# Kernel optimization log

Hardware: AMD Instinct MI355X
Metric: run time of the kernel (lower is better)

Reference implementation:

```python
import jax, jax.numpy as jnp
import numpy as np

NUM_HEADS = 12

def setup_inputs() -> dict:
    key = jax.random.key(0)
    ks = jax.random.split(key, 6)
    B, N, C, P = 16, 785, 768, 48
    return {
        "x": jax.random.normal(ks[0], (B, N, C), jnp.float32),
        "qkv_w": jax.random.normal(ks[1], (3 * C, C), jnp.float32) * 0.02,
        "pos_emb": jax.random.normal(ks[2], (N, N, P), jnp.float32) * 0.02,
        "pos_proj_w": jax.random.normal(ks[3], (NUM_HEADS, P), jnp.float32) * 0.02,
        "proj_w": jax.random.normal(ks[4], (C, C), jnp.float32) * 0.02,
        "proj_b": jnp.zeros((C,), jnp.float32),
    }

def reference(x, qkv_w, pos_emb, pos_proj_w, proj_w, proj_b):
    B, N, C = x.shape
    H = NUM_HEADS
    hd = C // H
    scale = hd ** -0.5
    # qkv projection: [B,N,3C] -> q,k,v each [B,H,N,hd]
    qkv = (x @ qkv_w.T).reshape(B, N, 3, H, hd)
    qkv = jnp.transpose(qkv, (2, 0, 3, 1, 4))
    q, k, v = qkv[0], qkv[1], qkv[2]
    # learned relative-position bias: [H,N,N]
    pos_score = jnp.einsum('nmp,hp->hnm', pos_emb, pos_proj_w)
    # attention scores: scale applied AFTER adding bias (matches original)
    attn = (jnp.einsum('bhnd,bhmd->bhnm', q, k) + pos_score[None]) * scale
    attn = jax.nn.softmax(attn, axis=-1)
    out = jnp.einsum('bhnm,bhmd->bhnd', attn, v)
    out = jnp.transpose(out, (0, 2, 1, 3)).reshape(B, N, C)
    return out @ proj_w.T + proj_b
```

## Files before the change

### kernel.cpp

```cpp
#include <hip/hip_runtime.h>
#include <hip/hip_fp16.h>

#define B_ 16
#define N_ 785
#define C_ 768
#define H_ 12
#define HD_ 64
#define P_ 48
#define M_ (B_*N_)
#define POSW 832
#define VTW  832
#define SLOG2E 0.1803368801111244f

#define OFF_Q   0
#define OFF_K   9646080
#define OFF_VT  19292160
#define OFF_POS 29515776
#define OFF_XF  37353216
#define OFF_AO  OFF_XF
#define OFF_WQ  47085312
#define OFF_WP  48854784

struct __align__(16) Half8 { __half h[8]; };
typedef _Float16 half8_t __attribute__((ext_vector_type(8)));
typedef _Float16 half4_t __attribute__((ext_vector_type(4)));
typedef float f32x4 __attribute__((ext_vector_type(4)));

__device__ __forceinline__ void gl16(const void* g, void* l) {
    __builtin_amdgcn_global_load_lds(
        (const __attribute__((address_space(1))) void*)g,
        (__attribute__((address_space(3))) void*)l, 16, 0, 0);
}

__device__ __forceinline__ int xcd_swz(int o, int nwg) {
    const int q = nwg >> 3, r = nwg & 7;
    const int xcd = o & 7, idx = o >> 3;
    const int base = xcd < r ? xcd * (q + 1) : r * (q + 1) + (xcd - r) * q;
    return base + idx;
}

#define NX4 2411520
#define NQ4 442368
#define NP4 147456
#define NTOT4 (NX4+NQ4+NP4)

__global__ __launch_bounds__(256) void convert_f16(
    const float* __restrict__ x, const float* __restrict__ wq,
    const float* __restrict__ wp, _Float16* __restrict__ xo,
    _Float16* __restrict__ wqo, _Float16* __restrict__ wpo)
{
    int i = blockIdx.x * 256 + threadIdx.x;
    const float4* s; _Float16* d; int o;
    if (i < NX4)            { s = (const float4*)x;  d = xo;  o = i; }
    else if (i < NX4 + NQ4) { s = (const float4*)wq; d = wqo; o = i - NX4; }
    else                    { s = (const float4*)wp; d = wpo; o = i - NX4 - NQ4; }
    float4 v = s[o];
    half4_t h = { (_Float16)v.x, (_Float16)v.y, (_Float16)v.z, (_Float16)v.w };
    *(half4_t*)&d[o * 4] = h;
}

#define QKV_NWG (18 * 99)

__global__ __launch_bounds__(256) void qkv_gemm_mfma(
    const _Float16* __restrict__ A, const _Float16* __restrict__ Bw,
    __half* __restrict__ qh, __half* __restrict__ kh, __half* __restrict__ vth)
{
    __shared__ _Float16 Asl[2][128 * 32];
    __shared__ _Float16 Bsl[2][128 * 32];

    const int t  = threadIdx.x;
    const int w  = t >> 6;
    const int l  = t & 63;
    const int lr = l & 15;
    const int lg = l >> 4;
    const int wm = (w >> 1) * 64;
    const int wn = (w & 1) * 64;

    const int g  = xcd_swz(blockIdx.x, QKV_NWG);
    const int nt = g % 18;
    const int n0 = nt * 128;
    const int m0 = (g / 18) * 128;

    const int f1 = t + 256;
    const int ar0 = t >> 2,  ac0 = (t & 3) * 8;
    const int ar1 = f1 >> 2, ac1 = (f1 & 3) * 8;
    const _Float16* Ag0 = A  + (size_t)(m0 + ar0) * 768 + ac0;
    const _Float16* Ag1 = A  + (size_t)(m0 + ar1) * 768 + ac1;
    const _Float16* Bg0 = Bw + (size_t)(n0 + ar0) * 768 + ac0;
    const _Float16* Bg1 = Bw + (size_t)(n0 + ar1) * 768 + ac1;

    f32x4 acc[4][4];
    #pragma unroll
    for (int i = 0; i < 4; ++i)
        #pragma unroll
        for (int j = 0; j < 4; ++j) acc[i][j] = (f32x4){0.f, 0.f, 0.f, 0.f};

    gl16(Ag0, &Asl[0][t * 8]); gl16(Ag1, &Asl[0][f1 * 8]);
    gl16(Bg0, &Bsl[0][t * 8]); gl16(Bg1, &Bsl[0][f1 * 8]);
    __syncthreads();

    #pragma unroll 2
    for (int it = 0; it < 24; ++it) {
        const int cur = it & 1;
        if (it < 23) {
            const int kn = (it + 1) * 32;
            gl16(Ag0 + kn, &Asl[cur ^ 1][t * 8]); gl16(Ag1 + kn, &Asl[cur ^ 1][f1 * 8]);
            gl16(Bg0 + kn, &Bsl[cur ^ 1][t * 8]); gl16(Bg1 + kn, &Bsl[cur ^ 1][f1 * 8]);
        }
        half8_t af[4], bf[4];
        #pragma unroll
        for (int i = 0; i < 4; ++i)
            af[i] = *(const half8_t*)&Asl[cur][(wm + i * 16 + lr) * 32 + lg * 8];
        #pragma unroll
        for (int j = 0; j < 4; ++j)
            bf[j] = *(const half8_t*)&Bsl[cur][(wn + j * 16 + lr) * 32 + lg * 8];
        __builtin_amdgcn_s_setprio(1);
        #pragma unroll
        for (int i = 0; i < 4; ++i)
            #pragma unroll
            for (int j = 0; j < 4; ++j)
                acc[i][j] = __builtin_amdgcn_mfma_f32_16x16x32_f16(af[i], bf[j], acc[i][j], 0, 0, 0);
        __builtin_amdgcn_s_setprio(0);
        __syncthreads();
    }

    const int tsel  = nt / 6;
    const int nbase = n0 - tsel * 768;
    #pragma unroll
    for (int i = 0; i < 4; ++i) {
        #pragma unroll
        for (int r = 0; r < 4; ++r) {
            const int m = m0 + wm + i * 16 + lg * 4 + r;
            if (m >= M_) continue;
            const int bb = m / N_, nn = m - bb * N_;
            #pragma unroll
            for (int j = 0; j < 4; ++j) {
                const int nsec = nbase + wn + j * 16 + lr;
                const int hh = nsec >> 6, dd = nsec & 63;
                const float v = acc[i][j][r];
                if (tsel == 0)
                    qh[((size_t)(bb * H_ + hh) * N_ + nn) * HD_ + dd] = __float2half(v * SLOG2E);
                else if (tsel == 1)
                    kh[((size_t)(bb * H_ + hh) * N_ + nn) * HD_ + dd] = __float2half(v);
                else
                    vth[((size_t)(bb * H_ + hh) * HD_ + dd) * VTW + nn] = __float2half(v);
            }
        }
    }
}

__global__ __launch_bounds__(256) void pos_kernel(
    const float* __restrict__ pe, const float* __restrict__ pw,
    __half* __restrict__ posh)
{
    __shared__ float W[H_][P_];
    const int t = threadIdx.x;
    for (int i = t; i < H_ * P_; i += 256) W[i / P_][i % P_] = pw[i];
    __syncthreads();
    int nm = blockIdx.x * 256 + t;
    if (nm >= N_ * N_) return;
    float e[48];
    const float4* src = (const float4*)(pe + (size_t)nm * 48);
    #pragma unroll
    for (int i = 0; i < 12; ++i) {
        float4 v = src[i];
        e[4*i] = v.x; e[4*i+1] = v.y; e[4*i+2] = v.z; e[4*i+3] = v.w;
    }
    int n = nm / N_, m = nm - n * N_;
    #pragma unroll
    for (int hh = 0; hh < H_; ++hh) {
        float s = 0.f;
        #pragma unroll
        for (int p = 0; p < 48; ++p) s = fmaf(e[p], W[hh][p], s);
        posh[((size_t)hh * N_ + n) * POSW + m] = __float2half(s * SLOG2E);
    }
}

#define NQT 13
#define ATT_NWG (192 * NQT)

__global__ __launch_bounds__(256) void attn_mfma(
    const _Float16* __restrict__ qh, const _Float16* __restrict__ kh,
    const _Float16* __restrict__ vt, const _Float16* __restrict__ posh,
    _Float16* __restrict__ aoh)
{
    __shared__ _Float16 Kl[64][72];
    __shared__ _Float16 Vl[64][72];
    __shared__ _Float16 Bl[64][72];

    const int t  = threadIdx.x;
    const int w  = t >> 6;
    const int l  = t & 63;
    const int lr = l & 15;
    const int lg = l >> 4;

    const int g2   = xcd_swz(blockIdx.x, ATT_NWG);
    const int qt   = g2 % NQT;
    const int rest = g2 / NQT;
    const int b    = rest & 15;
    const int h    = rest >> 4;
    const int bh   = b * H_ + h;
    const int n0   = qt * 64;

    const int qrow = n0 + w * 16 + lr;
    const int qrc  = qrow < N_ ? qrow : N_ - 1;
    const _Float16* qbase = qh + ((size_t)bh * N_ + qrc) * HD_;
    const half8_t qf0 = *(const half8_t*)(qbase + lg * 8);
    const half8_t qf1 = *(const half8_t*)(qbase + 32 + lg * 8);

    f32x4 O0 = {0.f,0.f,0.f,0.f}, O1 = O0, O2 = O0, O3 = O0;
    float m_run = -1e30f;
    float l_run = 0.f;

    const int srow = t >> 2;
    const int scol = (t & 3) * 16;
    const _Float16* kRow = kh + ((size_t)bh * N_) * HD_ + scol;
    const _Float16* vRow = vt + ((size_t)bh * HD_ + srow) * VTW + scol;
    const _Float16* bRow = posh + ((size_t)h * N_ + (n0 + srow < N_ ? n0 + srow : N_ - 1)) * POSW + scol;

    half8_t rk0, rk1, rv0, rv1, rb0, rb1;
    {
        const int gm = srow < N_ ? srow : N_ - 1;
        const half8_t* ks = (const half8_t*)(kRow + (size_t)gm * HD_);
        rk0 = ks[0]; rk1 = ks[1];
        const half8_t* vs = (const half8_t*)vRow;
        rv0 = vs[0]; rv1 = vs[1];
        const half8_t* bs = (const half8_t*)bRow;
        rb0 = bs[0]; rb1 = bs[1];
    }

    for (int c = 0; c < 13; ++c) {
        *(half8_t*)&Kl[srow][scol]     = rk0;
        *(half8_t*)&Kl[srow][scol + 8] = rk1;
        *(half8_t*)&Vl[srow][scol]     = rv0;
        *(half8_t*)&Vl[srow][scol + 8] = rv1;
        *(half8_t*)&Bl[srow][scol]     = rb0;
        *(half8_t*)&Bl[srow][scol + 8] = rb1;
        __syncthreads();

        if (c < 12) {
            const int m0n = (c + 1) * 64;
            const int gm  = (m0n + srow) < N_ ? (m0n + srow) : N_ - 1;
            const half8_t* ks = (const half8_t*)(kRow + (size_t)gm * HD_);
            rk0 = ks[0]; rk1 = ks[1];
            const half8_t* vs = (const half8_t*)(vRow + m0n);
            rv0 = vs[0]; rv1 = vs[1];
            const half8_t* bs = (const half8_t*)(bRow + m0n);
            rb0 = bs[0]; rb1 = bs[1];
        }

        f32x4 s[4];
        __builtin_amdgcn_s_setprio(1);
        #pragma unroll
        for (int ms = 0; ms < 4; ++ms) {
            half4_t b4 = *(const half4_t*)&Bl[w * 16 + lr][ms * 16 + lg * 4];
            f32x4 acc = { (float)b4[0], (float)b4[1], (float)b4[2], (float)b4[3] };
            half8_t k0 = *(const half8_t*)&Kl[ms * 16 + lr][lg * 8];
            half8_t k1 = *(const half8_t*)&Kl[ms * 16 + lr][32 + lg * 8];
            acc = __builtin_amdgcn_mfma_f32_16x16x32_f16(k0, qf0, acc, 0, 0, 0);
            acc = __builtin_amdgcn_mfma_f32_16x16x32_f16(k1, qf1, acc, 0, 0, 0);
            s[ms] = acc;
        }
        __builtin_amdgcn_s_setprio(0);

        if (c == 12) {
            #pragma unroll
            for (int ms = 0; ms < 4; ++ms)
                #pragma unroll
                for (int r = 0; r < 4; ++r)
                    if (ms * 16 + lg * 4 + r >= 17) s[ms][r] = -1e30f;
        }

        float x0 = fmaxf(fmaxf(s[0][0], s[0][1]), s[0][2]);
        float x1 = fmaxf(fmaxf(s[0][3], s[1][0]), s[1][1]);
        float x2 = fmaxf(fmaxf(s[1][2], s[1][3]), s[2][0]);
        float x3 = fmaxf(fmaxf(s[2][1], s[2][2]), s[2][3]);
        float x4 = fmaxf(fmaxf(s[3][0], s[3][1]), s[3][2]);
        float smax = fmaxf(fmaxf(fmaxf(x0, x1), x2),
                           fmaxf(fmaxf(x3, x4), s[3][3]));
        smax = fmaxf(smax, __shfl_xor(smax, 16));
        smax = fmaxf(smax, __shfl_xor(smax, 32));

        if (__any(smax > m_run + 8.f)) {
            const float mn    = fmaxf(m_run, smax);
            const float alpha = exp2f(m_run - mn);
            m_run = mn;
            l_run *= alpha;
            const float a0 = __shfl(alpha, lg * 4 + 0);
            const float a1 = __shfl(alpha, lg * 4 + 1);
            const float a2 = __shfl(alpha, lg * 4 + 2);
            const float a3 = __shfl(alpha, lg * 4 + 3);
            O0[0]*=a0; O0[1]*=a1; O0[2]*=a2; O0[3]*=a3;
            O1[0]*=a0; O1[1]*=a1; O1[2]*=a2; O1[3]*=a3;
            O2[0]*=a0; O2[1]*=a1; O2[2]*=a2; O2[3]*=a3;
            O3[0]*=a0; O3[1]*=a1; O3[2]*=a2; O3[3]*=a3;
        }

        float p[4][4];
        float psum = 0.f;
        #pragma unroll
        for (int ms = 0; ms < 4; ++ms)
            #pragma unroll
            for (int r = 0; r < 4; ++r) {
                p[ms][r] = exp2f(s[ms][r] - m_run);
                psum += p[ms][r];
            }
        psum += __shfl_xor(psum, 16);
        psum += __shfl_xor(psum, 32);
        l_run += psum;

        half8_t pa0 = { (_Float16)p[0][0], (_Float16)p[0][1], (_Float16)p[0][2], (_Float16)p[0][3],
                        (_Float16)p[1][0], (_Float16)p[1][1], (_Float16)p[1][2], (_Float16)p[1][3] };
        half8_t pa1 = { (_Float16)p[2][0], (_Float16)p[2][1], (_Float16)p[2][2], (_Float16)p[2][3],
                        (_Float16)p[3][0], (_Float16)p[3][1], (_Float16)p[3][2], (_Float16)p[3][3] };

        __builtin_amdgcn_s_setprio(1);
        #pragma unroll
        for (int ds = 0; ds < 4; ++ds) {
            const _Float16* vr = &Vl[ds * 16 + lr][0];
            half4_t v00 = *(const half4_t*)&vr[lg * 4];
            half4_t v01 = *(const half4_t*)&vr[16 + lg * 4];
            half4_t v10 = *(const half4_t*)&vr[32 + lg * 4];
            half4_t v11 = *(const half4_t*)&vr[48 + lg * 4];
            half8_t vf0 = __builtin_shufflevector(v00, v01, 0, 1, 2, 3, 4, 5, 6, 7);
            half8_t vf1 = __builtin_shufflevector(v10, v11, 0, 1, 2, 3, 4, 5, 6, 7);
            f32x4& Od = (ds == 0 ? O0 : ds == 1 ? O1 : ds == 2 ? O2 : O3);
            Od = __builtin_amdgcn_mfma_f32_16x16x32_f16(pa0, vf0, Od, 0, 0, 0);
            Od = __builtin_amdgcn_mfma_f32_16x16x32_f16(pa1, vf1, Od, 0, 0, 0);
        }
        __builtin_amdgcn_s_setprio(0);
        __syncthreads();
    }

    const int bb = bh / H_;
    #pragma unroll
    for (int r = 0; r < 4; ++r) {
        const int n = n0 + w * 16 + lg * 4 + r;
        if (n >= N_) continue;
        const float lv  = __shfl(l_run, lg * 4 + r);
        const float inv = 1.f / lv;
        _Float16* dst = aoh + ((size_t)(bb * N_ + n)) * C_ + h * HD_;
        dst[0 * 16 + lr] = (_Float16)(O0[r] * inv);
        dst[1 * 16 + lr] = (_Float16)(O1[r] * inv);
        dst[2 * 16 + lr] = (_Float16)(O2[r] * inv);
        dst[3 * 16 + lr] = (_Float16)(O3[r] * inv);
    }
}

#define PROJ_NWG (6 * 99)

__global__ __launch_bounds__(256) void proj_gemm_mfma(
    const _Float16* __restrict__ A, const _Float16* __restrict__ Bw,
    const float* __restrict__ bias, float* __restrict__ out)
{
    __shared__ _Float16 Asl[2][128 * 32];
    __shared__ _Float16 Bsl[2][128 * 32];

    const int t  = threadIdx.x;
    const int w  = t >> 6;
    const int l  = t & 63;
    const int lr = l & 15;
    const int lg = l >> 4;
    const int wm = (w >> 1) * 64;
    const int wn = (w & 1) * 64;

    const int g  = xcd_swz(blockIdx.x, PROJ_NWG);
    const int n0 = (g % 6) * 128;
    const int m0 = (g / 6) * 128;

    const int f1 = t + 256;
    const int ar0 = t >> 2,  ac0 = (t & 3) * 8;
    const int ar1 = f1 >> 2, ac1 = (f1 & 3) * 8;
    const _Float16* Ag0 = A  + (size_t)(m0 + ar0) * 768 + ac0;
    const _Float16* Ag1 = A  + (size_t)(m0 + ar1) * 768 + ac1;
    const _Float16* Bg0 = Bw + (size_t)(n0 + ar0) * 768 + ac0;
    const _Float16* Bg1 = Bw + (size_t)(n0 + ar1) * 768 + ac1;

    f32x4 acc[4][4];
    #pragma unroll
    for (int i = 0; i < 4; ++i)
        #pragma unroll
        for (int j = 0; j < 4; ++j) acc[i][j] = (f32x4){0.f, 0.f, 0.f, 0.f};

    gl16(Ag0, &Asl[0][t * 8]); gl16(Ag1, &Asl[0][f1 * 8]);
    gl16(Bg0, &Bsl[0][t * 8]); gl16(Bg1, &Bsl[0][f1 * 8]);
    __syncthreads();

    #pragma unroll 2
    for (int it = 0; it < 24; ++it) {
        const int cur = it & 1;
        if (it < 23) {
            const int kn = (it + 1) * 32;
            gl16(Ag0 + kn, &Asl[cur ^ 1][t * 8]); gl16(Ag1 + kn, &Asl[cur ^ 1][f1 * 8]);
            gl16(Bg0 + kn, &Bsl[cur ^ 1][t * 8]); gl16(Bg1 + kn, &Bsl[cur ^ 1][f1 * 8]);
        }
        half8_t af[4], bf[4];
        #pragma unroll
        for (int i = 0; i < 4; ++i)
            af[i] = *(const half8_t*)&Asl[cur][(wm + i * 16 + lr) * 32 + lg * 8];
        #pragma unroll
        for (int j = 0; j < 4; ++j)
            bf[j] = *(const half8_t*)&Bsl[cur][(wn + j * 16 + lr) * 32 + lg * 8];
        __builtin_amdgcn_s_setprio(1);
        #pragma unroll
        for (int i = 0; i < 4; ++i)
            #pragma unroll
            for (int j = 0; j < 4; ++j)
                acc[i][j] = __builtin_amdgcn_mfma_f32_16x16x32_f16(af[i], bf[j], acc[i][j], 0, 0, 0);
        __builtin_amdgcn_s_setprio(0);
        __syncthreads();
    }

    float bj[4];
    #pragma unroll
    for (int j = 0; j < 4; ++j) bj[j] = bias[n0 + wn + j * 16 + lr];
    #pragma unroll
    for (int i = 0; i < 4; ++i) {
        #pragma unroll
        for (int r = 0; r < 4; ++r) {
            const int m = m0 + wm + i * 16 + lg * 4 + r;
            if (m >= M_) continue;
            #pragma unroll
            for (int j = 0; j < 4; ++j) {
                const int n = n0 + wn + j * 16 + lr;
                out[(size_t)m * 768 + n] = acc[i][j][r] + bj[j];
            }
        }
    }
}

extern "C" void kernel_launch(void* const* d_in, const int* in_sizes, int n_in,
                              void* d_out, int out_size, void* d_ws, size_t ws_size,
                              hipStream_t stream)
{
    const float* x     = (const float*)d_in[0];
    const float* qkv_w = (const float*)d_in[1];
    const float* pe    = (const float*)d_in[2];
    const float* pw    = (const float*)d_in[3];
    const float* pjw   = (const float*)d_in[4];
    const float* pjb   = (const float*)d_in[5];
    float* out = (float*)d_out;

    _Float16* wsh  = (_Float16*)d_ws;
    _Float16* qh   = wsh + OFF_Q;
    _Float16* kh   = wsh + OFF_K;
    _Float16* vth  = wsh + OFF_VT;
    _Float16* posh = wsh + OFF_POS;
    _Float16* xf   = wsh + OFF_XF;
    _Float16* aoh  = wsh + OFF_AO;
    _Float16* wqf  = wsh + OFF_WQ;
    _Float16* wpf  = wsh + OFF_WP;

    convert_f16<<<dim3(NTOT4 / 256), 256, 0, stream>>>(x, qkv_w, pjw, xf, wqf, wpf);
    qkv_gemm_mfma<<<dim3(QKV_NWG), 256, 0, stream>>>(
        xf, wqf, (__half*)qh, (__half*)kh, (__half*)vth);
    pos_kernel<<<dim3((N_ * N_ + 255) / 256), 256, 0, stream>>>(pe, pw, (__half*)posh);
    attn_mfma<<<dim3(ATT_NWG), 256, 0, stream>>>(qh, kh, vth, posh, aoh);
    proj_gemm_mfma<<<dim3(PROJ_NWG), 256, 0, stream>>>(aoh, wpf, pjb, out);
}
```

Measured before the change: 275.6 us.

## Split attention key tiles across waves and store V row-major

Reorganizes the attention kernel so each wave handles a 16-key slice of every 64-key tile for all 64 queries, rather than 16 queries against all keys. Each wave keeps its own softmax max and sum plus partial outputs, and these are merged at the end through shared memory with per-wave rescaling and serialized accumulation. V is now written in row-major [bh,N,hd] layout instead of transposed, which removes the strided transposed stores in the QKV GEMM epilogue. The cost is more accumulator registers, strided scalar LDS reads for the V fragments, use of the smaller 16x16x16 MFMA, and an extra cross-wave reduction pass.

```diff
diff --git a/kernel.cpp b/kernel.cpp
--- a/kernel.cpp
+++ b/kernel.cpp
@@ -9,12 +9,11 @@
 #define P_ 48
 #define M_ (B_*N_)
 #define POSW 832
-#define VTW  832
 #define SLOG2E 0.1803368801111244f
 
 #define OFF_Q   0
 #define OFF_K   9646080
-#define OFF_VT  19292160
+#define OFF_V   19292160
 #define OFF_POS 29515776
 #define OFF_XF  37353216
 #define OFF_AO  OFF_XF
@@ -63,7 +62,7 @@
 
 __global__ __launch_bounds__(256) void qkv_gemm_mfma(
     const _Float16* __restrict__ A, const _Float16* __restrict__ Bw,
-    __half* __restrict__ qh, __half* __restrict__ kh, __half* __restrict__ vth)
+    __half* __restrict__ qh, __half* __restrict__ kh, __half* __restrict__ vh)
 {
     __shared__ _Float16 Asl[2][128 * 32];
     __shared__ _Float16 Bsl[2][128 * 32];
@@ -138,12 +137,10 @@
                 const int nsec = nbase + wn + j * 16 + lr;
                 const int hh = nsec >> 6, dd = nsec & 63;
                 const float v = acc[i][j][r];
-                if (tsel == 0)
-                    qh[((size_t)(bb * H_ + hh) * N_ + nn) * HD_ + dd] = __float2half(v * SLOG2E);
-                else if (tsel == 1)
-                    kh[((size_t)(bb * H_ + hh) * N_ + nn) * HD_ + dd] = __float2half(v);
-                else
-                    vth[((size_t)(bb * H_ + hh) * HD_ + dd) * VTW + nn] = __float2half(v);
+                const size_t dst = ((size_t)(bb * H_ + hh) * N_ + nn) * HD_ + dd;
+                if (tsel == 0)      qh[dst] = __float2half(v * SLOG2E);
+                else if (tsel == 1) kh[dst] = __float2half(v);
+                else                vh[dst] = __float2half(v);
             }
         }
     }
@@ -181,12 +178,16 @@
 
 __global__ __launch_bounds__(256) void attn_mfma(
     const _Float16* __restrict__ qh, const _Float16* __restrict__ kh,
-    const _Float16* __restrict__ vt, const _Float16* __restrict__ posh,
+    const _Float16* __restrict__ vh, const _Float16* __restrict__ posh,
     _Float16* __restrict__ aoh)
 {
-    __shared__ _Float16 Kl[64][72];
-    __shared__ _Float16 Vl[64][72];
-    __shared__ _Float16 Bl[64][72];
+    __shared__ __align__(16) char smem[28672];
+    _Float16 (*Kl)[72] = (_Float16 (*)[72])(smem);
+    _Float16 (*Vl)[72] = (_Float16 (*)[72])(smem + 9216);
+    _Float16 (*Bl)[72] = (_Float16 (*)[72])(smem + 18432);
+    float    (*Ol)[68] = (float (*)[68])(smem);
+    float*    Ml       = (float*)(smem + 17408);
+    float*    Ll       = (float*)(smem + 18432);
 
     const int t  = threadIdx.x;
     const int w  = t >> 6;
@@ -202,28 +203,35 @@
     const int bh   = b * H_ + h;
     const int n0   = qt * 64;
 
-    const int qrow = n0 + w * 16 + lr;
-    const int qrc  = qrow < N_ ? qrow : N_ - 1;
-    const _Float16* qbase = qh + ((size_t)bh * N_ + qrc) * HD_;
-    const half8_t qf0 = *(const half8_t*)(qbase + lg * 8);
-    const half8_t qf1 = *(const half8_t*)(qbase + 32 + lg * 8);
-
-    f32x4 O0 = {0.f,0.f,0.f,0.f}, O1 = O0, O2 = O0, O3 = O0;
-    float m_run = -1e30f;
-    float l_run = 0.f;
+    half8_t Qf0[4], Qf1[4];
+    #pragma unroll
+    for (int qg = 0; qg < 4; ++qg) {
+        const int qr = min(n0 + qg * 16 + lr, N_ - 1);
+        const _Float16* qb = qh + ((size_t)bh * N_ + qr) * HD_;
+        Qf0[qg] = *(const half8_t*)(qb + lg * 8);
+        Qf1[qg] = *(const half8_t*)(qb + 32 + lg * 8);
+    }
+
+    f32x4 O[4][4];
+    #pragma unroll
+    for (int qg = 0; qg < 4; ++qg)
+        #pragma unroll
+        for (int ds = 0; ds < 4; ++ds) O[qg][ds] = (f32x4){0.f, 0.f, 0.f, 0.f};
+    float m_r[4] = {-1e30f, -1e30f, -1e30f, -1e30f};
+    float lp[4]  = {0.f, 0.f, 0.f, 0.f};
 
     const int srow = t >> 2;
     const int scol = (t & 3) * 16;
     const _Float16* kRow = kh + ((size_t)bh * N_) * HD_ + scol;
-    const _Float16* vRow = vt + ((size_t)bh * HD_ + srow) * VTW + scol;
-    const _Float16* bRow = posh + ((size_t)h * N_ + (n0 + srow < N_ ? n0 + srow : N_ - 1)) * POSW + scol;
+    const _Float16* vRow = vh + ((size_t)bh * N_) * HD_ + scol;
+    const _Float16* bRow = posh + ((size_t)h * N_ + min(n0 + srow, N_ - 1)) * POSW + scol;
 
     half8_t rk0, rk1, rv0, rv1, rb0, rb1;
     {
-        const int gm = srow < N_ ? srow : N_ - 1;
+        const int gm = min(srow, N_ - 1);
         const half8_t* ks = (const half8_t*)(kRow + (size_t)gm * HD_);
         rk0 = ks[0]; rk1 = ks[1];
-        const half8_t* vs = (const half8_t*)vRow;
+        const half8_t* vs = (const half8_t*)(vRow + (size_t)gm * HD_);
         rv0 = vs[0]; rv1 = vs[1];
         const half8_t* bs = (const half8_t*)bRow;
         rb0 = bs[0]; rb1 = bs[1];
@@ -240,110 +248,141 @@
 
         if (c < 12) {
             const int m0n = (c + 1) * 64;
-            const int gm  = (m0n + srow) < N_ ? (m0n + srow) : N_ - 1;
+            const int gm  = min(m0n + srow, N_ - 1);
             const half8_t* ks = (const half8_t*)(kRow + (size_t)gm * HD_);
             rk0 = ks[0]; rk1 = ks[1];
-            const half8_t* vs = (const half8_t*)(vRow + m0n);
+            const half8_t* vs = (const half8_t*)(vRow + (size_t)gm * HD_);
             rv0 = vs[0]; rv1 = vs[1];
             const half8_t* bs = (const half8_t*)(bRow + m0n);
             rb0 = bs[0]; rb1 = bs[1];
         }
 
+        const half8_t k0 = *(const half8_t*)&Kl[w * 16 + lr][lg * 8];
+        const half8_t k1 = *(const half8_t*)&Kl[w * 16 + lr][32 + lg * 8];
         f32x4 s[4];
         __builtin_amdgcn_s_setprio(1);
         #pragma unroll
-        for (int ms = 0; ms < 4; ++ms) {
-            half4_t b4 = *(const half4_t*)&Bl[w * 16 + lr][ms * 16 + lg * 4];
+        for (int qg = 0; qg < 4; ++qg) {
+            half4_t b4 = *(const half4_t*)&Bl[qg * 16 + lr][w * 16 + lg * 4];
             f32x4 acc = { (float)b4[0], (float)b4[1], (float)b4[2], (float)b4[3] };
-            half8_t k0 = *(const half8_t*)&Kl[ms * 16 + lr][lg * 8];
-            half8_t k1 = *(const half8_t*)&Kl[ms * 16 + lr][32 + lg * 8];
-            acc = __builtin_amdgcn_mfma_f32_16x16x32_f16(k0, qf0, acc, 0, 0, 0);
-            acc = __builtin_amdgcn_mfma_f32_16x16x32_f16(k1, qf1, acc, 0, 0, 0);
-            s[ms] = acc;
+            acc = __builtin_amdgcn_mfma_f32_16x16x32_f16(k0, Qf0[qg], acc, 0, 0, 0);
+            acc = __builtin_amdgcn_mfma_f32_16x16x32_f16(k1, Qf1[qg], acc, 0, 0, 0);
+            s[qg] = acc;
         }
         __builtin_amdgcn_s_setprio(0);
 
         if (c == 12) {
             #pragma unroll
-            for (int ms = 0; ms < 4; ++ms)
+            for (int qg = 0; qg < 4; ++qg)
                 #pragma unroll
                 for (int r = 0; r < 4; ++r)
-                    if (ms * 16 + lg * 4 + r >= 17) s[ms][r] = -1e30f;
-        }
-
-        float x0 = fmaxf(fmaxf(s[0][0], s[0][1]), s[0][2]);
-        float x1 = fmaxf(fmaxf(s[0][3], s[1][0]), s[1][1]);
-        float x2 = fmaxf(fmaxf(s[1][2], s[1][3]), s[2][0]);
-        float x3 = fmaxf(fmaxf(s[2][1], s[2][2]), s[2][3]);
-        float x4 = fmaxf(fmaxf(s[3][0], s[3][1]), s[3][2]);
-        float smax = fmaxf(fmaxf(fmaxf(x0, x1), x2),
-                           fmaxf(fmaxf(x3, x4), s[3][3]));
-        smax = fmaxf(smax, __shfl_xor(smax, 16));
-        smax = fmaxf(smax, __shfl_xor(smax, 32));
-
-        if (__any(smax > m_run + 8.f)) {
-            const float mn    = fmaxf(m_run, smax);
-            const float alpha = exp2f(m_run - mn);
-            m_run = mn;
-            l_run *= alpha;
-            const float a0 = __shfl(alpha, lg * 4 + 0);
-            const float a1 = __shfl(alpha, lg * 4 + 1);
-            const float a2 = __shfl(alpha, lg * 4 + 2);
-            const float a3 = __shfl(alpha, lg * 4 + 3);
-            O0[0]*=a0; O0[1]*=a1; O0[2]*=a2; O0[3]*=a3;
-            O1[0]*=a0; O1[1]*=a1; O1[2]*=a2; O1[3]*=a3;
-            O2[0]*=a0; O2[1]*=a1; O2[2]*=a2; O2[3]*=a3;
-            O3[0]*=a0; O3[1]*=a1; O3[2]*=a2; O3[3]*=a3;
-        }
-
-        float p[4][4];
-        float psum = 0.f;
-        #pragma unroll
-        for (int ms = 0; ms < 4; ++ms)
-            #pragma unroll
-            for (int r = 0; r < 4; ++r) {
-                p[ms][r] = exp2f(s[ms][r] - m_run);
-                psum += p[ms][r];
+                    if (w * 16 + lg * 4 + r >= 17) s[qg][r] = -1e30f;
+        }
+
+        float mq[4];
+        #pragma unroll
+        for (int qg = 0; qg < 4; ++qg)
+            mq[qg] = fmaxf(fmaxf(s[qg][0], s[qg][1]), fmaxf(s[qg][2], s[qg][3]));
+        const bool trig = (mq[0] > m_r[0] + 8.f) || (mq[1] > m_r[1] + 8.f) ||
+                          (mq[2] > m_r[2] + 8.f) || (mq[3] > m_r[3] + 8.f);
+        if (__any(trig)) {
+            #pragma unroll
+            for (int qg = 0; qg < 4; ++qg) {
+                float v = fmaxf(mq[qg], __shfl_xor(mq[qg], 16));
+                v = fmaxf(v, __shfl_xor(v, 32));
+                const float mn = fmaxf(m_r[qg], v);
+                const float al = exp2f(m_r[qg] - mn);
+                m_r[qg] = mn;
+                lp[qg] *= al;
+                f32x4 av;
+                #pragma unroll
+                for (int r = 0; r < 4; ++r) av[r] = __shfl(al, lg * 4 + r);
+                #pragma unroll
+                for (int ds = 0; ds < 4; ++ds) O[qg][ds] *= av;
             }
-        psum += __shfl_xor(psum, 16);
-        psum += __shfl_xor(psum, 32);
-        l_run += psum;
-
-        half8_t pa0 = { (_Float16)p[0][0], (_Float16)p[0][1], (_Float16)p[0][2], (_Float16)p[0][3],
-                        (_Float16)p[1][0], (_Float16)p[1][1], (_Float16)p[1][2], (_Float16)p[1][3] };
-        half8_t pa1 = { (_Float16)p[2][0], (_Float16)p[2][1], (_Float16)p[2][2], (_Float16)p[2][3],
-                        (_Float16)p[3][0], (_Float16)p[3][1], (_Float16)p[3][2], (_Float16)p[3][3] };
+        }
+
+        half4_t pf[4];
+        #pragma unroll
+        for (int qg = 0; qg < 4; ++qg) {
+            float p0 = exp2f(s[qg][0] - m_r[qg]);
+            float p1 = exp2f(s[qg][1] - m_r[qg]);
+            float p2 = exp2f(s[qg][2] - m_r[qg]);
+            float p3 = exp2f(s[qg][3] - m_r[qg]);
+            lp[qg] += (p0 + p1) + (p2 + p3);
+            pf[qg] = (half4_t){ (_Float16)p0, (_Float16)p1, (_Float16)p2, (_Float16)p3 };
+        }
 
         __builtin_amdgcn_s_setprio(1);
         #pragma unroll
         for (int ds = 0; ds < 4; ++ds) {
-            const _Float16* vr = &Vl[ds * 16 + lr][0];
-            half4_t v00 = *(const half4_t*)&vr[lg * 4];
-            half4_t v01 = *(const half4_t*)&vr[16 + lg * 4];
-            half4_t v10 = *(const half4_t*)&vr[32 + lg * 4];
-            half4_t v11 = *(const half4_t*)&vr[48 + lg * 4];
-            half8_t vf0 = __builtin_shufflevector(v00, v01, 0, 1, 2, 3, 4, 5, 6, 7);
-            half8_t vf1 = __builtin_shufflevector(v10, v11, 0, 1, 2, 3, 4, 5, 6, 7);
-            f32x4& Od = (ds == 0 ? O0 : ds == 1 ? O1 : ds == 2 ? O2 : O3);
-            Od = __builtin_amdgcn_mfma_f32_16x16x32_f16(pa0, vf0, Od, 0, 0, 0);
-            Od = __builtin_amdgcn_mfma_f32_16x16x32_f16(pa1, vf1, Od, 0, 0, 0);
+            half4_t vb;
+            #pragma unroll
+            for (int i = 0; i < 4; ++i)
+                vb[i] = Vl[w * 16 + lg * 4 + i][ds * 16 + lr];
+            #pragma unroll
+            for (int qg = 0; qg < 4; ++qg)
+                O[qg][ds] = __builtin_amdgcn_mfma_f32_16x16x16f16(pf[qg], vb, O[qg][ds], 0, 0, 0);
         }
         __builtin_amdgcn_s_setprio(0);
         __syncthreads();
     }
 
-    const int bb = bh / H_;
-    #pragma unroll
-    for (int r = 0; r < 4; ++r) {
-        const int n = n0 + w * 16 + lg * 4 + r;
-        if (n >= N_) continue;
-        const float lv  = __shfl(l_run, lg * 4 + r);
-        const float inv = 1.f / lv;
-        _Float16* dst = aoh + ((size_t)(bb * N_ + n)) * C_ + h * HD_;
-        dst[0 * 16 + lr] = (_Float16)(O0[r] * inv);
-        dst[1 * 16 + lr] = (_Float16)(O1[r] * inv);
-        dst[2 * 16 + lr] = (_Float16)(O2[r] * inv);
-        dst[3 * 16 + lr] = (_Float16)(O3[r] * inv);
+    if (lg == 0) {
+        #pragma unroll
+        for (int qg = 0; qg < 4; ++qg) Ml[w * 64 + qg * 16 + lr] = m_r[qg];
+    }
+    __syncthreads();
+    f32x4 av[4];
+    #pragma unroll
+    for (int qg = 0; qg < 4; ++qg) {
+        const int q = qg * 16 + lr;
+        const float mt = fmaxf(fmaxf(Ml[q], Ml[64 + q]), fmaxf(Ml[128 + q], Ml[192 + q]));
+        const float aw = exp2f(m_r[qg] - mt);
+        float lw = lp[qg] * aw;
+        lw += __shfl_xor(lw, 16);
+        lw += __shfl_xor(lw, 32);
+        if (lg == 0) Ll[w * 64 + q] = lw;
+        #pragma unroll
+        for (int r = 0; r < 4; ++r) av[qg][r] = __shfl(aw, lg * 4 + r);
+    }
+    #pragma unroll
+    for (int wp = 0; wp < 4; ++wp) {
+        __syncthreads();
+        if (w == wp) {
+            #pragma unroll
+            for (int qg = 0; qg < 4; ++qg)
+                #pragma unroll
+                for (int ds = 0; ds < 4; ++ds)
+                    #pragma unroll
+                    for (int r = 0; r < 4; ++r) {
+                        const float val = O[qg][ds][r] * av[qg][r];
+                        float* slot = &Ol[qg * 16 + lg * 4 + r][ds * 16 + lr];
+                        if (wp == 0) *slot = val;
+                        else         *slot += val;
+                    }
+        }
+    }
+    __syncthreads();
+
+    {
+        const int q  = t >> 2;
+        const int dg = (t & 3) * 16;
+        const int n  = n0 + q;
+        if (n < N_) {
+            const float lt = Ll[q] + Ll[64 + q] + Ll[128 + q] + Ll[192 + q];
+            const float inv = 1.f / lt;
+            const float* src = &Ol[q][dg];
+            half8_t o0, o1;
+            #pragma unroll
+            for (int e = 0; e < 8; ++e) {
+                o0[e] = (_Float16)(src[e] * inv);
+                o1[e] = (_Float16)(src[8 + e] * inv);
+            }
+            _Float16* dst = aoh + ((size_t)((bh / H_) * N_ + n)) * C_ + h * HD_ + dg;
+            *(half8_t*)dst = o0;
+            *(half8_t*)(dst + 8) = o1;
+        }
     }
 }
 
@@ -444,7 +483,7 @@
     _Float16* wsh  = (_Float16*)d_ws;
     _Float16* qh   = wsh + OFF_Q;
     _Float16* kh   = wsh + OFF_K;
-    _Float16* vth  = wsh + OFF_VT;
+    _Float16* vh   = wsh + OFF_V;
     _Float16* posh = wsh + OFF_POS;
     _Float16* xf   = wsh + OFF_XF;
     _Float16* aoh  = wsh + OFF_AO;
@@ -453,8 +492,8 @@
 
     convert_f16<<<dim3(NTOT4 / 256), 256, 0, stream>>>(x, qkv_w, pjw, xf, wqf, wpf);
     qkv_gemm_mfma<<<dim3(QKV_NWG), 256, 0, stream>>>(
-        xf, wqf, (__half*)qh, (__half*)kh, (__half*)vth);
+        xf, wqf, (__half*)qh, (__half*)kh, (__half*)vh);
     pos_kernel<<<dim3((N_ * N_ + 255) / 256), 256, 0, stream>>>(pe, pw, (__half*)posh);
-    attn_mfma<<<dim3(ATT_NWG), 256, 0, stream>>>(qh, kh, vth, posh, aoh);
+    attn_mfma<<<dim3(ATT_NWG), 256, 0, stream>>>(qh, kh, vh, posh, aoh);
     proj_gemm_mfma<<<dim3(PROJ_NWG), 256, 0, stream>>>(aoh, wpf, pjb, out);
 }
```

New measurement: 344.1 us. +24.9%, slower.
